# Kernel tuning notes

Hardware: AMD Instinct MI355X
Metric: run time of the kernel (lower is better)

The kernel has to match this reference:

```python
import jax, jax.numpy as jnp
import numpy as np

N, C, T, V = 8, 256, 256, 25
NH = 8
DK = 256           # dk_factor(1.0) * out_channels
DV = 256           # only_temporal_attention -> dv = out_channels
DKH = DK // NH     # 32
DVH = DV // NH     # 32
BN_EPS = 1e-5


def setup_inputs() -> dict:
    key = jax.random.key(0)
    ks = jax.random.split(key, 10)
    return {
        "x": jax.random.normal(ks[0], (N, C, T, V), jnp.float32),
        # pointwise (1,1) qkv conv: weight (2*dk+dv, C), torch conv_init scale
        "qkv_w": jax.random.normal(ks[1], (2 * DK + DV, C), jnp.float32) * (2.0 / (2 * DK + DV)) ** 0.5,
        "qkv_b": jax.random.normal(ks[2], (2 * DK + DV,), jnp.float32) * 0.02,
        # relative key embeddings: (2*frames-1, dk // Nh)
        "key_rel": jax.random.normal(ks[3], (2 * T - 1, DKH), jnp.float32),
        # attn_out pointwise conv: (dv, dv)
        "attn_w": jax.random.normal(ks[4], (DV, DV), jnp.float32) * (1.0 / DV) ** 0.5,
        "attn_b": jax.random.normal(ks[5], (DV,), jnp.float32) * 0.02,
        # BatchNorm2d (eval mode) params / running stats
        "bn_gamma": 1.0 + 0.1 * jax.random.normal(ks[6], (DV,), jnp.float32),
        "bn_beta": 0.1 * jax.random.normal(ks[7], (DV,), jnp.float32),
        "bn_mean": 0.1 * jax.random.normal(ks[8], (DV,), jnp.float32),
        "bn_var": jax.random.uniform(ks[9], (DV,), jnp.float32, minval=0.5, maxval=1.5),
    }


def rel_to_abs(x):
    # x: (B, Nh, L, 2L-1) -> (B, Nh, L, L) via standard pad/reshape/slice trick
    B, Nh, L, _ = x.shape
    x = jnp.pad(x, ((0, 0), (0, 0), (0, 0), (0, 1)))          # (B,Nh,L,2L)
    flat = x.reshape(B, Nh, L * 2 * L)
    flat = jnp.pad(flat, ((0, 0), (0, 0), (0, L - 1)))
    final = flat.reshape(B, Nh, L + 1, 2 * L - 1)
    return final[:, :, :L, L - 1:]


def reference(x, qkv_w, qkv_b, key_rel, attn_w, attn_b, bn_gamma, bn_beta, bn_mean, bn_var):
    n, c, t, v = x.shape
    x_sum = x
    B = n * v
    # (N,C,T,V) -> (N*V, C, T): each joint is an independent temporal sequence
    xr = jnp.transpose(x, (0, 3, 1, 2)).reshape(B, c, t)
    # pointwise qkv conv (kernel (1,1), stride 1)
    qkv = jnp.einsum('bct,oc->bot', xr, qkv_w) + qkv_b[None, :, None]
    q, k, vv = qkv[:, :DK], qkv[:, DK:2 * DK], qkv[:, 2 * DK:]
    q = q.reshape(B, NH, DKH, t) * (DKH ** -0.5)   # scaling applied before rel logits too
    k = k.reshape(B, NH, DKH, t)
    vv = vv.reshape(B, NH, DVH, t)
    # content logits: (B,NH,t,t)
    logits = jnp.einsum('bhdt,bhds->bhts', q, k)
    # relative logits: (B,NH,t,2t-1) -> abs (B,NH,t,t)
    rel = jnp.einsum('bhdt,md->bhtm', q, key_rel)
    logits = logits + rel_to_abs(rel)
    weights = jax.nn.softmax(logits, axis=-1)
    attn = jnp.einsum('bhts,bhds->bhtd', weights, vv)          # (B,NH,t,DVH)
    # combine heads (head-major channel order) -> (B, DV, t)
    attn = jnp.transpose(attn, (0, 1, 3, 2)).reshape(B, DV, t)
    # attn_out pointwise conv
    attn = jnp.einsum('bct,oc->bot', attn, attn_w) + attn_b[None, :, None]
    # (N*V, DV, T) -> (N, DV, T, V)
    attn = attn.reshape(n, v, DV, t).transpose(0, 2, 3, 1)
    # skip connection (in==out, stride==1 -> identity down path)
    result = attn + x_sum
    # BatchNorm2d in eval mode
    inv = bn_gamma / jnp.sqrt(bn_var + BN_EPS)
    result = result * inv[None, :, None, None] + (bn_beta - bn_mean * inv)[None, :, None, None]
    return jax.nn.relu(result)
```

## Files before the change

kernel.cpp:

```cpp
#include <hip/hip_runtime.h>
#include <stdint.h>

#define NB 8
#define CC 256
#define TT 256
#define VV 25

typedef unsigned int u32;
typedef unsigned short u16;
typedef __attribute__((ext_vector_type(8))) short s16x8;
typedef __attribute__((ext_vector_type(4))) float f32x4;

__device__ __forceinline__ float bf2f(u16 u) { return __uint_as_float((u32)u << 16); }
__device__ __forceinline__ u16 f2bf(float f) {
    u32 u = __float_as_uint(f);
    u += 0x7fffu + ((u >> 16) & 1u);
    return (u16)(u >> 16);
}

__device__ __forceinline__ void gload_lds16(const void* g, void* l) {
    __builtin_amdgcn_global_load_lds(
        (const __attribute__((address_space(1))) u32*)g,
        (__attribute__((address_space(3))) u32*)l, 16, 0, 0);
}

__global__ __launch_bounds__(256) void k_transpose_x(const float* __restrict__ x,
                                                     u16* __restrict__ xT) {
    __shared__ u16 L[25 * 32 * 34];
    const int tid = threadIdx.x;
    const int c0 = blockIdx.x * 32;
    const int t0 = blockIdx.y * 32;
    const int n  = blockIdx.z;
    for (int i = tid; i < 25600; i += 256) {
        int ci = i / 800;
        int rem = i - ci * 800;
        int t = rem / 25;
        int v = rem - t * 25;
        float f = x[(((size_t)(n * CC + c0 + ci)) * TT + t0) * VV + rem];
        L[(v * 32 + t) * 34 + ci] = f2bf(f);
    }
    __syncthreads();
    for (int i = tid; i < 12800; i += 256) {
        int row = i >> 4, cp = i & 15;
        int v = row >> 5, t = row & 31;
        u32 val = *(const u32*)&L[row * 34 + cp * 2];
        *(u32*)&xT[(((size_t)(n * VV + v)) * TT + t0 + t) * CC + c0 + cp * 2] = val;
    }
}

__global__ __launch_bounds__(256) void k_pack_krel(const float* __restrict__ kr,
                                                   u16* __restrict__ krb) {
    int g = blockIdx.x * 256 + threadIdx.x;
    if (g >= 16384) return;
    krb[g] = (g < 511 * 32) ? f2bf(kr[g]) : (u16)0;
}

__global__ __launch_bounds__(256) void k_pack_w(const float* __restrict__ qkv_w,
                                                const float* __restrict__ attn_w,
                                                const float* __restrict__ qkv_b,
                                                u16* __restrict__ Wqk,
                                                u16* __restrict__ Wv,
                                                u16* __restrict__ Wo,
                                                float* __restrict__ bqk) {
    const float s = 0.17677669529663687f * 1.4426950408889634f;
    int g = blockIdx.x * 256 + threadIdx.x;
    if (g < 131072) {
        Wqk[g] = f2bf(qkv_w[g] * (g < 65536 ? s : 1.f));
    } else if (g < 196608) {
        Wv[g - 131072] = f2bf(qkv_w[g]);
    } else if (g < 262144) {
        Wo[g - 196608] = f2bf(attn_w[g - 196608]);
    } else if (g < 262656) {
        int i = g - 262144;
        bqk[i] = qkv_b[i] * (i < 256 ? s : 1.f);
    }
}

__device__ __forceinline__ void gemm_mainloop(const u16* __restrict__ Arow,
                                              const u16* __restrict__ Brow,
                                              u16* At, u16* Bt,
                                              int wave, int lane, f32x4 acc[4][4]) {
    const int srow = lane >> 2, scol = (lane & 3) * 8;
    const int quad = lane >> 4, l15 = lane & 15;
    for (int k0 = 0; k0 < 256; k0 += 32) {
#pragma unroll
        for (int it = 0; it < 2; ++it) {
            int ch = it * 4 + wave;
            gload_lds16(Arow + (size_t)(ch * 16 + srow) * 256 + k0 + scol, At + ch * 512 + lane * 8);
            gload_lds16(Brow + (size_t)(ch * 16 + srow) * 256 + k0 + scol, Bt + ch * 512 + lane * 8);
        }
        __syncthreads();
        s16x8 af[4], bfr[4];
#pragma unroll
        for (int i = 0; i < 4; ++i)
            af[i] = *(const s16x8*)&At[((wave & 1) * 64 + i * 16 + l15) * 32 + quad * 8];
#pragma unroll
        for (int j = 0; j < 4; ++j)
            bfr[j] = *(const s16x8*)&Bt[((wave >> 1) * 64 + j * 16 + l15) * 32 + quad * 8];
#pragma unroll
        for (int i = 0; i < 4; ++i)
#pragma unroll
            for (int j = 0; j < 4; ++j)
                acc[i][j] = __builtin_amdgcn_mfma_f32_16x16x32_bf16(af[i], bfr[j], acc[i][j], 0, 0, 0);
        __syncthreads();
    }
}

__global__ __launch_bounds__(256) void k_gemm_qk(const u16* __restrict__ xT,
                                                 const u16* __restrict__ Wqk,
                                                 const float* __restrict__ bqk,
                                                 u16* __restrict__ qT,
                                                 u16* __restrict__ kT) {
    __shared__ __align__(16) u16 At[128 * 32];
    __shared__ __align__(16) u16 Bt[128 * 32];
    const int tid = threadIdx.x, wave = tid >> 6, lane = tid & 63;
    const int quad = lane >> 4, l15 = lane & 15;
    const int n0 = blockIdx.x * 128;
    const int m0 = blockIdx.y * 128;
    const int b  = blockIdx.z;
    const u16* Arow = xT + (size_t)b * 65536 + (size_t)m0 * 256;
    const u16* Brow = Wqk + (size_t)n0 * 256;
    f32x4 acc[4][4];
#pragma unroll
    for (int i = 0; i < 4; ++i)
#pragma unroll
        for (int j = 0; j < 4; ++j) acc[i][j] = (f32x4){0.f, 0.f, 0.f, 0.f};
    gemm_mainloop(Arow, Brow, At, Bt, wave, lane, acc);

    const bool isq = (n0 < 256);
    u16* base = isq ? qT : kT;
    const int on0 = (isq ? n0 : n0 - 256) + (wave >> 1) * 64;
#pragma unroll
    for (int j = 0; j < 4; ++j) {
        int o = on0 + j * 16 + l15;
        float bias = bqk[(isq ? 0 : 256) + o];
        u16* dcol = base + (size_t)(b * 8 + (o >> 5)) * 8192 + (o & 31);
#pragma unroll
        for (int i = 0; i < 4; ++i) {
            int tbase = m0 + (wave & 1) * 64 + i * 16 + quad * 4;
#pragma unroll
            for (int r = 0; r < 4; ++r)
                dcol[(size_t)(tbase + r) * 32] = f2bf(acc[i][j][r] + bias);
        }
    }
}

__global__ __launch_bounds__(256) void k_gemm_av(const u16* __restrict__ Wb,
                                                 const float* __restrict__ bias,
                                                 const u16* __restrict__ Bsrc,
                                                 u16* __restrict__ Out) {
    __shared__ __align__(16) u16 At[128 * 32];
    __shared__ __align__(16) u16 Bt[128 * 32];
    const int tid = threadIdx.x, wave = tid >> 6, lane = tid & 63;
    const int quad = lane >> 4, l15 = lane & 15;
    const int n0 = blockIdx.x * 128;
    const int m0 = blockIdx.y * 128;
    const int b  = blockIdx.z;
    const u16* Arow = Wb + (size_t)m0 * 256;
    const u16* Brow = Bsrc + (size_t)b * 65536 + (size_t)n0 * 256;
    f32x4 acc[4][4];
#pragma unroll
    for (int i = 0; i < 4; ++i)
#pragma unroll
        for (int j = 0; j < 4; ++j) acc[i][j] = (f32x4){0.f, 0.f, 0.f, 0.f};
    gemm_mainloop(Arow, Brow, At, Bt, wave, lane, acc);

    u16* ob = Out + (size_t)b * 65536;
    const int nb = n0 + (wave >> 1) * 64 + l15;
#pragma unroll
    for (int i = 0; i < 4; ++i) {
        int o_i = m0 + (wave & 1) * 64 + i * 16 + quad * 4;
#pragma unroll
        for (int r = 0; r < 4; ++r) {
            float bv = bias[o_i + r];
            u16* orow = ob + (size_t)(o_i + r) * 256 + nb;
#pragma unroll
            for (int j = 0; j < 4; ++j)
                orow[j * 16] = f2bf(acc[i][j][r] + bv);
        }
    }
}

__global__ __launch_bounds__(256, 4) void k_attention_mfma(const u16* __restrict__ qT,
                                                           const u16* __restrict__ kT,
                                                           const u16* __restrict__ vb,
                                                           const u16* __restrict__ krb,
                                                           u16* __restrict__ attn) {
    __shared__ __align__(16) u16 RP[4][16 * 280];

    const int tid = threadIdx.x;
    const int bx = blockIdx.x;
    const int xcd = bx & 7;
    const int ii  = bx >> 3;
    const int bh  = xcd * 200 + (ii >> 2);
    const int tt  = ii & 3;
    const int b = bh >> 3, h = bh & 7;
    const int wave = tid >> 6, lane = tid & 63;
    const int quad = lane >> 4, l15 = lane & 15;
    const int t0w = tt * 64 + wave * 16;
    const int tl = quad * 4;

    u16* rp = &RP[wave][0];
    const u16* qg  = qT  + (size_t)bh * 8192;
    const u16* kg  = kT  + (size_t)bh * 8192;
    const u16* vg  = vb  + (size_t)bh * 8192;
    const u16* krg = krb + (size_t)(240 - t0w) * 32;

    s16x8 afrag = *(const s16x8*)(qg + (size_t)(t0w + l15) * 32 + quad * 8);
    const f32x4 z4 = {0.f, 0.f, 0.f, 0.f};

    f32x4 acc[16];
    __builtin_amdgcn_s_setprio(1);
#pragma unroll
    for (int n = 0; n < 16; ++n) {
        s16x8 kf = *(const s16x8*)(kg + (size_t)(n * 16 + l15) * 32 + quad * 8);
        acc[n] = __builtin_amdgcn_mfma_f32_16x16x32_bf16(afrag, kf, z4, 0, 0, 0);
    }
    __builtin_amdgcn_s_setprio(0);

    int srcl[4];
    bool msrc[4];
#pragma unroll
    for (int r = 0; r < 4; ++r) {
        int K = 15 - tl - r;
        srcl[r] = quad * 16 + ((l15 + K) & 15);
        msrc[r] = l15 < K;
    }
    f32x4 rc = __builtin_amdgcn_mfma_f32_16x16x32_bf16(
        afrag, *(const s16x8*)(krg + (size_t)l15 * 32 + quad * 8), z4, 0, 0, 0);
#pragma unroll
    for (int n = 0; n < 16; ++n) {
        f32x4 rn = __builtin_amdgcn_mfma_f32_16x16x32_bf16(
            afrag, *(const s16x8*)(krg + (size_t)((n + 1) * 16 + l15) * 32 + quad * 8),
            z4, 0, 0, 0);
#pragma unroll
        for (int r = 0; r < 4; ++r) {
            float vsel = msrc[r] ? rn[r] : rc[r];
            acc[n][r] += __shfl(vsel, srcl[r], 64);
        }
        rc = rn;
    }

    float invr[4];
#pragma unroll
    for (int r = 0; r < 4; ++r) {
        float mr[8];
#pragma unroll
        for (int n = 0; n < 8; ++n) mr[n] = fmaxf(acc[n][r], acc[n + 8][r]);
#pragma unroll
        for (int n = 0; n < 4; ++n) mr[n] = fmaxf(mr[n], mr[n + 4]);
        float m = fmaxf(fmaxf(mr[0], mr[1]), fmaxf(mr[2], mr[3]));
#pragma unroll
        for (int off = 1; off < 16; off <<= 1) m = fmaxf(m, __shfl_xor(m, off, 64));
#pragma unroll
        for (int n = 0; n < 16; ++n) acc[n][r] = exp2f(acc[n][r] - m);
        float sr[8];
#pragma unroll
        for (int n = 0; n < 8; ++n) sr[n] = acc[n][r] + acc[n + 8][r];
#pragma unroll
        for (int n = 0; n < 4; ++n) sr[n] = sr[n] + sr[n + 4];
        float s = (sr[0] + sr[1]) + (sr[2] + sr[3]);
#pragma unroll
        for (int off = 1; off < 16; off <<= 1) s += __shfl_xor(s, off, 64);
        invr[r] = 1.f / s;
    }

#pragma unroll
    for (int n = 0; n < 16; ++n) {
#pragma unroll
        for (int r = 0; r < 4; ++r)
            rp[(tl + r) * 280 + n * 16 + l15] = f2bf(acc[n][r]);
    }

#pragma unroll
    for (int j = 0; j < 2; ++j) {
        f32x4 o = {0.f, 0.f, 0.f, 0.f};
        __builtin_amdgcn_s_setprio(1);
#pragma unroll
        for (int ks = 0; ks < 8; ++ks) {
            s16x8 a  = *(const s16x8*)&rp[l15 * 280 + ks * 32 + quad * 8];
            s16x8 bv = *(const s16x8*)(vg + (size_t)(j * 16 + l15) * 256 + ks * 32 + quad * 8);
            o = __builtin_amdgcn_mfma_f32_16x16x32_bf16(a, bv, o, 0, 0, 0);
        }
        __builtin_amdgcn_s_setprio(0);
        u16* ob = attn + ((size_t)b * 256 + t0w + tl) * 256 + h * 32 + j * 16 + l15;
        ob[0]   = f2bf(o[0] * invr[0]);
        ob[256] = f2bf(o[1] * invr[1]);
        ob[512] = f2bf(o[2] * invr[2]);
        ob[768] = f2bf(o[3] * invr[3]);
    }
}

__global__ __launch_bounds__(256) void k_final(const u16* __restrict__ y,
                                               const float* __restrict__ x,
                                               const float* __restrict__ gamma,
                                               const float* __restrict__ beta,
                                               const float* __restrict__ mean,
                                               const float* __restrict__ var,
                                               float* __restrict__ out) {
    __shared__ float tile[1600];
    const int tid = threadIdx.x;
    const int t0 = blockIdx.x * 64;
    const int o  = blockIdx.y;
    const int n  = blockIdx.z;
    float inv = gamma[o] * rsqrtf(var[o] + 1e-5f);
    float sh  = beta[o] - mean[o] * inv;
    for (int p = tid; p < 1600; p += 256) {
        int v = p >> 6, j = p & 63;
        tile[j * VV + v] = bf2f(y[(((size_t)(n * VV + v)) * CC + o) * TT + t0 + j]);
    }
    __syncthreads();
    size_t gbase = (((size_t)(n * CC + o)) * TT + t0) * VV;
    for (int i = tid; i < 1600; i += 256) {
        float val = tile[i] + x[gbase + i];
        val = val * inv + sh;
        out[gbase + i] = fmaxf(val, 0.f);
    }
}

extern "C" void kernel_launch(void* const* d_in, const int* in_sizes, int n_in,
                              void* d_out, int out_size, void* d_ws, size_t ws_size,
                              hipStream_t stream) {
    const float* x        = (const float*)d_in[0];
    const float* qkv_w    = (const float*)d_in[1];
    const float* qkv_b    = (const float*)d_in[2];
    const float* key_rel  = (const float*)d_in[3];
    const float* attn_w   = (const float*)d_in[4];
    const float* attn_b   = (const float*)d_in[5];
    const float* bn_gamma = (const float*)d_in[6];
    const float* bn_beta  = (const float*)d_in[7];
    const float* bn_mean  = (const float*)d_in[8];
    const float* bn_var   = (const float*)d_in[9];
    float* out = (float*)d_out;

    char* ws = (char*)d_ws;
    u16* xT    = (u16*)ws;
    u16* qT    = (u16*)(ws + 26214400);
    u16* kT    = (u16*)(ws + 52428800);
    u16* vb    = (u16*)(ws + 78643200);
    u16* attnT = (u16*)(ws + 104857600);
    u16* y     = qT;

    char* outc = (char*)d_out;
    u16* Wqk   = (u16*)outc;
    u16* Wv    = (u16*)(outc + 262144);
    u16* Wo    = (u16*)(outc + 393216);
    float* bqk = (float*)(outc + 524288);
    u16* krb   = (u16*)(outc + 526336);

    k_pack_w<<<1026, 256, 0, stream>>>(qkv_w, attn_w, qkv_b, Wqk, Wv, Wo, bqk);
    k_pack_krel<<<64, 256, 0, stream>>>(key_rel, krb);
    k_transpose_x<<<dim3(8, 8, 8), 256, 0, stream>>>(x, xT);
    k_gemm_qk<<<dim3(4, 2, 200), 256, 0, stream>>>(xT, Wqk, bqk, qT, kT);
    k_gemm_av<<<dim3(2, 2, 200), 256, 0, stream>>>(Wv, qkv_b + 512, xT, vb);
    k_attention_mfma<<<dim3(6400), 256, 0, stream>>>(qT, kT, vb, krb, attnT);
    k_gemm_av<<<dim3(2, 2, 200), 256, 0, stream>>>(Wo, attn_b, attnT, y);
    k_final<<<dim3(4, 256, 8), 256, 0, stream>>>(y, x, bn_gamma, bn_beta, bn_mean, bn_var, out);
}
```

Measured before the change: 347.1 us.

## Stage K, V and relative keys in LDS per block, chunk P·V

The attention kernel now loads each head's K, V and its block's slice of relative-key embeddings into shared memory once per block using global_load_lds. The four waves then read MFMA fragments from LDS instead of each wave fetching them from global memory. The probability-times-V step is also split into four chunks of 64 columns using a smaller per-wave P buffer, and both output halves are accumulated in one pass. This trades more LDS per block (about 60KB) and a block-wide barrier for less redundant global traffic, which may lower occupancy now that the launch-bounds minimum-block hint is removed.

```diff
diff --git a/kernel.cpp b/kernel.cpp
--- a/kernel.cpp
+++ b/kernel.cpp
@@ -181,12 +181,15 @@
     }
 }
 
-__global__ __launch_bounds__(256, 4) void k_attention_mfma(const u16* __restrict__ qT,
-                                                           const u16* __restrict__ kT,
-                                                           const u16* __restrict__ vb,
-                                                           const u16* __restrict__ krb,
-                                                           u16* __restrict__ attn) {
-    __shared__ __align__(16) u16 RP[4][16 * 280];
+__global__ __launch_bounds__(256) void k_attention_mfma(const u16* __restrict__ qT,
+                                                        const u16* __restrict__ kT,
+                                                        const u16* __restrict__ vb,
+                                                        const u16* __restrict__ krb,
+                                                        u16* __restrict__ attn) {
+    __shared__ __align__(16) u16 Kl[8192];
+    __shared__ __align__(16) u16 Vl[8192];
+    __shared__ __align__(16) u16 KRl[10240];
+    __shared__ __align__(16) u16 Pl[4][1152];
 
     const int tid = threadIdx.x;
     const int bx = blockIdx.x;
@@ -200,20 +203,38 @@
     const int t0w = tt * 64 + wave * 16;
     const int tl = quad * 4;
 
-    u16* rp = &RP[wave][0];
-    const u16* qg  = qT  + (size_t)bh * 8192;
-    const u16* kg  = kT  + (size_t)bh * 8192;
-    const u16* vg  = vb  + (size_t)bh * 8192;
-    const u16* krg = krb + (size_t)(240 - t0w) * 32;
+    const u16* qg  = qT + (size_t)bh * 8192;
+    const u16* kg  = kT + (size_t)bh * 8192;
+    const u16* vg  = vb + (size_t)bh * 8192;
+    const u16* krB = krb + (size_t)(192 - tt * 64) * 32;
 
     s16x8 afrag = *(const s16x8*)(qg + (size_t)(t0w + l15) * 32 + quad * 8);
+
+#pragma unroll
+    for (int i = 0; i < 4; ++i) {
+        int tk = i * 4 + wave;
+        gload_lds16(kg + (size_t)(tk * 16 + l15) * 32 + quad * 8, Kl + tk * 512 + lane * 8);
+    }
+#pragma unroll
+    for (int i = 0; i < 4; ++i) {
+        int f = i * 4 + wave;
+        gload_lds16(vg + (size_t)((f >> 3) * 16 + l15) * 256 + (f & 7) * 32 + quad * 8,
+                    Vl + f * 512 + lane * 8);
+    }
+#pragma unroll
+    for (int i = 0; i < 5; ++i) {
+        int tr = i * 4 + wave;
+        gload_lds16(krB + (size_t)(tr * 16 + l15) * 32 + quad * 8, KRl + tr * 512 + lane * 8);
+    }
+    __syncthreads();
+
     const f32x4 z4 = {0.f, 0.f, 0.f, 0.f};
 
     f32x4 acc[16];
     __builtin_amdgcn_s_setprio(1);
 #pragma unroll
     for (int n = 0; n < 16; ++n) {
-        s16x8 kf = *(const s16x8*)(kg + (size_t)(n * 16 + l15) * 32 + quad * 8);
+        s16x8 kf = *(const s16x8*)&Kl[n * 512 + lane * 8];
         acc[n] = __builtin_amdgcn_mfma_f32_16x16x32_bf16(afrag, kf, z4, 0, 0, 0);
     }
     __builtin_amdgcn_s_setprio(0);
@@ -226,13 +247,13 @@
         srcl[r] = quad * 16 + ((l15 + K) & 15);
         msrc[r] = l15 < K;
     }
+    const int tb = 3 - wave;
     f32x4 rc = __builtin_amdgcn_mfma_f32_16x16x32_bf16(
-        afrag, *(const s16x8*)(krg + (size_t)l15 * 32 + quad * 8), z4, 0, 0, 0);
+        afrag, *(const s16x8*)&KRl[tb * 512 + lane * 8], z4, 0, 0, 0);
 #pragma unroll
     for (int n = 0; n < 16; ++n) {
         f32x4 rn = __builtin_amdgcn_mfma_f32_16x16x32_bf16(
-            afrag, *(const s16x8*)(krg + (size_t)((n + 1) * 16 + l15) * 32 + quad * 8),
-            z4, 0, 0, 0);
+            afrag, *(const s16x8*)&KRl[(tb + n + 1) * 512 + lane * 8], z4, 0, 0, 0);
 #pragma unroll
         for (int r = 0; r < 4; ++r) {
             float vsel = msrc[r] ? rn[r] : rc[r];
@@ -265,30 +286,39 @@
         invr[r] = 1.f / s;
     }
 
-#pragma unroll
-    for (int n = 0; n < 16; ++n) {
-#pragma unroll
-        for (int r = 0; r < 4; ++r)
-            rp[(tl + r) * 280 + n * 16 + l15] = f2bf(acc[n][r]);
-    }
-
-#pragma unroll
-    for (int j = 0; j < 2; ++j) {
-        f32x4 o = {0.f, 0.f, 0.f, 0.f};
+    u16* pw = &Pl[wave][0];
+    f32x4 o0 = z4, o1 = z4;
+#pragma unroll
+    for (int c = 0; c < 4; ++c) {
+#pragma unroll
+        for (int nn = 0; nn < 4; ++nn) {
+            int n = c * 4 + nn;
+#pragma unroll
+            for (int r = 0; r < 4; ++r)
+                pw[(tl + r) * 72 + nn * 16 + l15] = f2bf(acc[n][r]);
+        }
         __builtin_amdgcn_s_setprio(1);
 #pragma unroll
-        for (int ks = 0; ks < 8; ++ks) {
-            s16x8 a  = *(const s16x8*)&rp[l15 * 280 + ks * 32 + quad * 8];
-            s16x8 bv = *(const s16x8*)(vg + (size_t)(j * 16 + l15) * 256 + ks * 32 + quad * 8);
-            o = __builtin_amdgcn_mfma_f32_16x16x32_bf16(a, bv, o, 0, 0, 0);
+        for (int kk = 0; kk < 2; ++kk) {
+            int ks = c * 2 + kk;
+            s16x8 a  = *(const s16x8*)&pw[l15 * 72 + kk * 32 + quad * 8];
+            s16x8 v0 = *(const s16x8*)&Vl[ks * 512 + lane * 8];
+            s16x8 v1 = *(const s16x8*)&Vl[(8 + ks) * 512 + lane * 8];
+            o0 = __builtin_amdgcn_mfma_f32_16x16x32_bf16(a, v0, o0, 0, 0, 0);
+            o1 = __builtin_amdgcn_mfma_f32_16x16x32_bf16(a, v1, o1, 0, 0, 0);
         }
         __builtin_amdgcn_s_setprio(0);
-        u16* ob = attn + ((size_t)b * 256 + t0w + tl) * 256 + h * 32 + j * 16 + l15;
-        ob[0]   = f2bf(o[0] * invr[0]);
-        ob[256] = f2bf(o[1] * invr[1]);
-        ob[512] = f2bf(o[2] * invr[2]);
-        ob[768] = f2bf(o[3] * invr[3]);
-    }
+    }
+
+    u16* ob = attn + ((size_t)b * 256 + t0w + tl) * 256 + h * 32 + l15;
+    ob[0]        = f2bf(o0[0] * invr[0]);
+    ob[256]      = f2bf(o0[1] * invr[1]);
+    ob[512]      = f2bf(o0[2] * invr[2]);
+    ob[768]      = f2bf(o0[3] * invr[3]);
+    ob[16]       = f2bf(o1[0] * invr[0]);
+    ob[256 + 16] = f2bf(o1[1] * invr[1]);
+    ob[512 + 16] = f2bf(o1[2] * invr[2]);
+    ob[768 + 16] = f2bf(o1[3] * invr[3]);
 }
 
 __global__ __launch_bounds__(256) void k_final(const u16* __restrict__ y,
```

Result: faster. 332.8 us (-4.1%).
